# Optimization experiments

Measured on AMD Instinct MI355X. Metric: run time of the kernel, lower is better.

The kernel has to match this reference:

```python
import jax, jax.numpy as jnp
import numpy as np

HIDDEN = 2048
NUM_HEADS = 32
GROUP_SIZE = 4
HEAD_DIM = HIDDEN // NUM_HEADS            # 64
GROUP_NUM = NUM_HEADS // GROUP_SIZE       # 8 KV heads
B, S = 2, 2048


def setup_inputs() -> dict:
    key = jax.random.key(0)
    ks = jax.random.split(key, 7)
    sc = 1.0 / np.sqrt(HIDDEN)
    x = jax.random.normal(ks[0], (B, S, HIDDEN), dtype=jnp.float32)
    attention_mask = jnp.ones((B, S), dtype=jnp.int32)
    Wq = jax.random.normal(ks[1], (HIDDEN, HIDDEN), dtype=jnp.float32) * sc
    bq = jax.random.normal(ks[2], (HIDDEN,), dtype=jnp.float32) * 0.02
    Wk = jax.random.normal(ks[3], (HIDDEN, GROUP_NUM * HEAD_DIM), dtype=jnp.float32) * sc
    bk = jax.random.normal(ks[4], (GROUP_NUM * HEAD_DIM,), dtype=jnp.float32) * 0.02
    Wv = jax.random.normal(ks[5], (HIDDEN, GROUP_NUM * HEAD_DIM), dtype=jnp.float32) * sc
    bv = jax.random.normal(ks[6], (GROUP_NUM * HEAD_DIM,), dtype=jnp.float32) * 0.02
    return {"x": x, "attention_mask": attention_mask,
            "Wq": Wq, "bq": bq, "Wk": Wk, "bk": bk, "Wv": Wv, "bv": bv}


def reference(x, attention_mask, Wq, bq, Wk, bk, Wv, bv):
    b, s, _ = x.shape
    # projections
    q = (x @ Wq + bq).reshape(b, s, NUM_HEADS, HEAD_DIM).transpose(0, 2, 1, 3)   # (B,H,S,hd)
    k = (x @ Wk + bk).reshape(b, s, GROUP_NUM, HEAD_DIM).transpose(0, 2, 1, 3)   # (B,G,S,hd)
    v = (x @ Wv + bv).reshape(b, s, GROUP_NUM, HEAD_DIM).transpose(0, 2, 1, 3)
    # expand KV groups to full head count (head h uses group h // group_size)
    k = jnp.repeat(k, GROUP_SIZE, axis=1)                                        # (B,H,S,hd)
    v = jnp.repeat(v, GROUP_SIZE, axis=1)
    # NOTE: original torch code uses floor-division `//` for scaling and no softmax
    score = jnp.floor(jnp.einsum('bhqd,bhkd->bhqk', q, k) / np.sqrt(HEAD_DIM).astype(np.float32))
    score = jnp.where(attention_mask[:, None, None, :] == 0, -jnp.inf, score)
    out = jnp.einsum('bhqk,bhkd->bhqd', score, v)                                # (B,H,S,hd)
    return out.transpose(0, 2, 1, 3).reshape(b, s, HIDDEN)
```

## Files before the change

### kernel.cpp

```cpp
#include <hip/hip_runtime.h>
#include <math.h>

#define HIDDEN 2048
#define NHEADS 32
#define HDIM 64
#define GNUM 8
#define KVDIM 512
#define BB 2
#define SS 2048
#define MROWS (BB * SS)
#define NQKV 3072

typedef _Float16 half8 __attribute__((ext_vector_type(8)));
typedef _Float16 half4 __attribute__((ext_vector_type(4)));
typedef _Float16 half2 __attribute__((ext_vector_type(2)));
typedef float floatx4 __attribute__((ext_vector_type(4)));

#define MFMA16(a, b, c) __builtin_amdgcn_mfma_f32_16x16x32_f16((a), (b), (c), 0, 0, 0)

__device__ __forceinline__ void split_f32(float x, _Float16& hi, _Float16& lo) {
    hi = (_Float16)x;
    lo = (_Float16)((x - (float)hi) * 2048.0f);
}

__device__ __forceinline__ void load_lds16(const void* g, void* l) {
    __builtin_amdgcn_global_load_lds(
        (const __attribute__((address_space(1))) void*)g,
        (__attribute__((address_space(3))) void*)l, 16, 0, 0);
}

__global__ __launch_bounds__(256)
void split_x(const float* __restrict__ x, _Float16* __restrict__ xh,
             _Float16* __restrict__ xl, int n4) {
    for (int idx = blockIdx.x * 256 + threadIdx.x; idx < n4; idx += gridDim.x * 256) {
        floatx4 v = reinterpret_cast<const floatx4*>(x)[idx];
        half4 h, l;
        #pragma unroll
        for (int e = 0; e < 4; ++e) { _Float16 hi, lo; split_f32(v[e], hi, lo); h[e] = hi; l[e] = lo; }
        reinterpret_cast<half4*>(xh)[idx] = h;
        reinterpret_cast<half4*>(xl)[idx] = l;
    }
}

__global__ __launch_bounds__(256)
void split_wt(const float* __restrict__ W, int N, int n0,
              _Float16* __restrict__ Wth, _Float16* __restrict__ Wtl) {
    __shared__ float tile[64][68];
    const int tid = threadIdx.x;
    const int kb = blockIdx.x, nb = blockIdx.y;
    #pragma unroll
    for (int i = 0; i < 4; ++i) {
        int idx = tid + i * 256;
        int r = idx >> 4, c4 = idx & 15;
        floatx4 v = *reinterpret_cast<const floatx4*>(&W[(size_t)(kb * 64 + r) * N + nb * 64 + c4 * 4]);
        *reinterpret_cast<floatx4*>(&tile[r][c4 * 4]) = v;
    }
    __syncthreads();
    #pragma unroll
    for (int i = 0; i < 4; ++i) {
        int idx = tid + i * 256;
        int r2 = idx >> 4, c2 = (idx & 15) * 4;
        half4 h, l;
        #pragma unroll
        for (int e = 0; e < 4; ++e) {
            _Float16 hi, lo;
            split_f32(tile[c2 + e][r2], hi, lo);
            h[e] = hi; l[e] = lo;
        }
        size_t o = (size_t)(n0 + nb * 64 + r2) * HIDDEN + kb * 64 + c2;
        *reinterpret_cast<half4*>(&Wth[o]) = h;
        *reinterpret_cast<half4*>(&Wtl[o]) = l;
    }
}

__global__ __launch_bounds__(256)
void biascat_k(const float* __restrict__ bq, const float* __restrict__ bk,
               const float* __restrict__ bv, float* __restrict__ bias) {
    int i = blockIdx.x * 256 + threadIdx.x;
    if (i < 2048) bias[i] = bq[i];
    else if (i < 2560) bias[i] = bk[i - 2048];
    else if (i < NQKV) bias[i] = bv[i - 2560];
}

__global__ __launch_bounds__(256, 2)
void gemm_qkv(const _Float16* __restrict__ xh, const _Float16* __restrict__ xl,
              const _Float16* __restrict__ Wth, const _Float16* __restrict__ Wtl,
              const float* __restrict__ bias,
              _Float16* __restrict__ qh, _Float16* __restrict__ ql,
              _Float16* __restrict__ kh, _Float16* __restrict__ kl,
              _Float16* __restrict__ vh) {
    __shared__ __align__(16) _Float16 Ah[128 * 64];
    __shared__ __align__(16) _Float16 Al[128 * 64];
    __shared__ __align__(16) _Float16 Bh[128 * 64];
    __shared__ __align__(16) _Float16 Bl[128 * 64];

    const int tid  = threadIdx.x;
    const int lane = tid & 63;
    const int w    = tid >> 6;
    const int wm   = w >> 1, wn = w & 1;
    const int bm   = blockIdx.x, bn = blockIdx.y;
    const int ml   = lane & 15;
    const int kg8  = (lane >> 4) * 8;

    const _Float16* gsrc;
    _Float16* ldst;
    if      (w == 0) { gsrc = xh  + (size_t)(bm * 128) * HIDDEN; ldst = Ah; }
    else if (w == 1) { gsrc = xl  + (size_t)(bm * 128) * HIDDEN; ldst = Al; }
    else if (w == 2) { gsrc = Wth + (size_t)(bn * 128) * HIDDEN; ldst = Bh; }
    else             { gsrc = Wtl + (size_t)(bn * 128) * HIDDEN; ldst = Bl; }

    floatx4 acc0[4][4] = {};
    floatx4 accL[4][4] = {};

    for (int k0 = 0; k0 < HIDDEN; k0 += 64) {
        #pragma unroll
        for (int i = 0; i < 16; ++i) {
            int L   = i * 1024 + lane * 16;
            int row = L >> 7;
            int off = (L & 127) ^ ((row & 7) << 4);
            const void* gp = (const char*)(gsrc + (size_t)row * HIDDEN + k0) + off;
            void* lp = (char*)ldst + i * 1024;
            load_lds16(gp, lp);
        }
        __syncthreads();

        #pragma unroll
        for (int kc = 0; kc < 2; ++kc) {
            half8 a_h[4], a_l[4], b_h[4], b_l[4];
            #pragma unroll
            for (int r = 0; r < 4; ++r) {
                int row = wm * 64 + r * 16 + ml;
                int byt = row * 128 + (((kc * 64 + kg8 * 2)) ^ ((row & 7) << 4));
                a_h[r] = *reinterpret_cast<const half8*>((const char*)Ah + byt);
                a_l[r] = *reinterpret_cast<const half8*>((const char*)Al + byt);
            }
            #pragma unroll
            for (int c = 0; c < 4; ++c) {
                int row = wn * 64 + c * 16 + ml;
                int byt = row * 128 + (((kc * 64 + kg8 * 2)) ^ ((row & 7) << 4));
                b_h[c] = *reinterpret_cast<const half8*>((const char*)Bh + byt);
                b_l[c] = *reinterpret_cast<const half8*>((const char*)Bl + byt);
            }
            #pragma unroll
            for (int r = 0; r < 4; ++r)
                #pragma unroll
                for (int c = 0; c < 4; ++c) {
                    acc0[r][c] = MFMA16(a_h[r], b_h[c], acc0[r][c]);
                    accL[r][c] = MFMA16(a_h[r], b_l[c], accL[r][c]);
                    accL[r][c] = MFMA16(a_l[r], b_h[c], accL[r][c]);
                }
        }
        __syncthreads();
    }

    #pragma unroll
    for (int c = 0; c < 4; ++c) {
        int colg = bn * 128 + wn * 64 + c * 16 + ml;
        float bval = bias[colg];
        #pragma unroll
        for (int r = 0; r < 4; ++r) {
            int rowg = bm * 128 + wm * 64 + r * 16 + (lane >> 4) * 4;
            #pragma unroll
            for (int reg = 0; reg < 4; ++reg) {
                float val = acc0[r][c][reg] + accL[r][c][reg] * (1.0f / 2048.0f) + bval;
                int rr = rowg + reg;
                if (colg < 2048) {
                    _Float16 hi, lo; split_f32(val, hi, lo);
                    qh[(size_t)rr * HIDDEN + colg] = hi;
                    ql[(size_t)rr * HIDDEN + colg] = lo;
                } else if (colg < 2560) {
                    int ck = colg - 2048;
                    _Float16 hi, lo; split_f32(val, hi, lo);
                    kh[(size_t)rr * KVDIM + ck] = hi;
                    kl[(size_t)rr * KVDIM + ck] = lo;
                } else {
                    vh[(size_t)rr * KVDIM + (colg - 2560)] = (_Float16)val;
                }
            }
        }
    }
}

__global__ __launch_bounds__(256, 2)
void attn4(const _Float16* __restrict__ qh, const _Float16* __restrict__ ql,
           const _Float16* __restrict__ kh, const _Float16* __restrict__ kl,
           const _Float16* __restrict__ vh, const int* __restrict__ mask,
           float* __restrict__ out) {
    __shared__ __align__(16) _Float16 Ksh[64][72];
    __shared__ __align__(16) _Float16 Ksl[64][72];
    __shared__ __align__(16) _Float16 Vst[64][72];
    __shared__ __align__(16) _Float16 Ss[4][4][16][72];

    const int tid  = threadIdx.x;
    const int lane = tid & 63;
    const int w    = tid >> 6;
    const int ml   = lane & 15;
    const int kg8  = (lane >> 4) * 8;
    const int qt   = blockIdx.x;
    const int b    = blockIdx.y >> 3, g = blockIdx.y & 7;

    half8 qhf[4][2], qlf[4][2];
    {
        size_t rowbase = (size_t)(b * SS + qt * 64 + w * 16 + ml) * HIDDEN;
        #pragma unroll
        for (int hh = 0; hh < 4; ++hh) {
            int hcol = (g * 4 + hh) * HDIM;
            #pragma unroll
            for (int gch = 0; gch < 2; ++gch) {
                qhf[hh][gch] = *reinterpret_cast<const half8*>(&qh[rowbase + hcol + gch * 32 + kg8]);
                qlf[hh][gch] = *reinterpret_cast<const half8*>(&ql[rowbase + hcol + gch * 32 + kg8]);
            }
        }
    }

    const _Float16* khg = kh + (size_t)b * SS * KVDIM + g * HDIM;
    const _Float16* klg = kl + (size_t)b * SS * KVDIM + g * HDIM;
    const _Float16* vhg = vh + (size_t)b * SS * KVDIM + g * HDIM;
    const int* mb = mask + b * SS;

    floatx4 oacc[4][4] = {};

    for (int kt = 0; kt < SS / 64; ++kt) {
        __syncthreads();
        #pragma unroll
        for (int i = 0; i < 2; ++i) {
            int idx = tid + i * 256;
            int kk = idx >> 3, d8 = (idx & 7) * 8;
            *reinterpret_cast<half8*>(&Ksh[kk][d8]) =
                *reinterpret_cast<const half8*>(&khg[(size_t)(kt * 64 + kk) * KVDIM + d8]);
            *reinterpret_cast<half8*>(&Ksl[kk][d8]) =
                *reinterpret_cast<const half8*>(&klg[(size_t)(kt * 64 + kk) * KVDIM + d8]);
        }
        {
            int rp = (tid & 31) * 2, c8 = (tid >> 5) * 8;
            half8 v0 = *reinterpret_cast<const half8*>(&vhg[(size_t)(kt * 64 + rp) * KVDIM + c8]);
            half8 v1 = *reinterpret_cast<const half8*>(&vhg[(size_t)(kt * 64 + rp + 1) * KVDIM + c8]);
            #pragma unroll
            for (int e = 0; e < 8; ++e)
                *reinterpret_cast<half2*>(&Vst[c8 + e][rp]) = half2{v0[e], v1[e]};
        }
        __syncthreads();

        int mv[4];
        #pragma unroll
        for (int fc = 0; fc < 4; ++fc) mv[fc] = mb[kt * 64 + fc * 16 + ml];

        #pragma unroll
        for (int fc = 0; fc < 4; ++fc) {
            half8 k_h[2], k_l[2];
            #pragma unroll
            for (int gch = 0; gch < 2; ++gch) {
                k_h[gch] = *reinterpret_cast<const half8*>(&Ksh[fc * 16 + ml][gch * 32 + kg8]);
                k_l[gch] = *reinterpret_cast<const half8*>(&Ksl[fc * 16 + ml][gch * 32 + kg8]);
            }
            #pragma unroll
            for (int hh = 0; hh < 4; ++hh) {
                floatx4 s0 = {}, sL = {};
                #pragma unroll
                for (int gch = 0; gch < 2; ++gch) {
                    s0 = MFMA16(qhf[hh][gch], k_h[gch], s0);
                    sL = MFMA16(qhf[hh][gch], k_l[gch], sL);
                    sL = MFMA16(qlf[hh][gch], k_h[gch], sL);
                }
                #pragma unroll
                for (int r = 0; r < 4; ++r) {
                    float sv = s0[r] + sL[r] * (1.0f / 2048.0f);
                    sv = floorf(sv * 0.125f);
                    if (mv[fc] == 0) sv = -INFINITY;
                    Ss[w][hh][(lane >> 4) * 4 + r][fc * 16 + ml] = (_Float16)sv;
                }
            }
        }

        half8 sa[4][2];
        #pragma unroll
        for (int hh = 0; hh < 4; ++hh)
            #pragma unroll
            for (int sg = 0; sg < 2; ++sg)
                sa[hh][sg] = *reinterpret_cast<const half8*>(&Ss[w][hh][ml][sg * 32 + kg8]);
        #pragma unroll
        for (int f = 0; f < 4; ++f) {
            half8 vb0 = *reinterpret_cast<const half8*>(&Vst[f * 16 + ml][kg8]);
            half8 vb1 = *reinterpret_cast<const half8*>(&Vst[f * 16 + ml][32 + kg8]);
            #pragma unroll
            for (int hh = 0; hh < 4; ++hh) {
                oacc[hh][f] = MFMA16(sa[hh][0], vb0, oacc[hh][f]);
                oacc[hh][f] = MFMA16(sa[hh][1], vb1, oacc[hh][f]);
            }
        }
    }

    #pragma unroll
    for (int hh = 0; hh < 4; ++hh) {
        int hcol = (g * 4 + hh) * HDIM;
        #pragma unroll
        for (int f = 0; f < 4; ++f)
            #pragma unroll
            for (int reg = 0; reg < 4; ++reg) {
                int row = b * SS + qt * 64 + w * 16 + (lane >> 4) * 4 + reg;
                out[(size_t)row * HIDDEN + hcol + f * 16 + ml] = oacc[hh][f][reg];
            }
    }
}

extern "C" void kernel_launch(void* const* d_in, const int* in_sizes, int n_in,
                              void* d_out, int out_size, void* d_ws, size_t ws_size,
                              hipStream_t stream) {
    (void)in_sizes; (void)n_in; (void)out_size; (void)ws_size;
    const float* x    = (const float*)d_in[0];
    const int*   mask = (const int*)d_in[1];
    const float* Wq   = (const float*)d_in[2];
    const float* bq   = (const float*)d_in[3];
    const float* Wk   = (const float*)d_in[4];
    const float* bk   = (const float*)d_in[5];
    const float* Wv   = (const float*)d_in[6];
    const float* bv   = (const float*)d_in[7];

    _Float16* ws16 = (_Float16*)d_ws;
    size_t o = 0;
    auto alloc16 = [&](size_t n) { _Float16* p = ws16 + o; o += n; return p; };
    _Float16* xh  = alloc16((size_t)MROWS * HIDDEN);
    _Float16* xl  = alloc16((size_t)MROWS * HIDDEN);
    _Float16* Wth = alloc16((size_t)NQKV * HIDDEN);
    _Float16* Wtl = alloc16((size_t)NQKV * HIDDEN);
    _Float16* qh  = alloc16((size_t)MROWS * HIDDEN);
    _Float16* ql  = alloc16((size_t)MROWS * HIDDEN);
    _Float16* kh  = alloc16((size_t)MROWS * KVDIM);
    _Float16* kl  = alloc16((size_t)MROWS * KVDIM);
    _Float16* vh  = alloc16((size_t)MROWS * KVDIM);
    float* biascat = (float*)(ws16 + o);

    split_x<<<2048, 256, 0, stream>>>(x, xh, xl, MROWS * HIDDEN / 4);
    split_wt<<<dim3(32, 32), 256, 0, stream>>>(Wq, HIDDEN, 0,    Wth, Wtl);
    split_wt<<<dim3(32, 8),  256, 0, stream>>>(Wk, KVDIM, 2048, Wth, Wtl);
    split_wt<<<dim3(32, 8),  256, 0, stream>>>(Wv, KVDIM, 2560, Wth, Wtl);
    biascat_k<<<12, 256, 0, stream>>>(bq, bk, bv, biascat);
    gemm_qkv<<<dim3(MROWS / 128, NQKV / 128), 256, 0, stream>>>(
        xh, xl, Wth, Wtl, biascat, qh, ql, kh, kl, vh);
    attn4<<<dim3(SS / 64, BB * GNUM), 256, 0, stream>>>(qh, ql, kh, kl, vh, mask, (float*)d_out);
}
```

Baseline: 336.8 us.

## Keep attention scores in registers via permlane swaps and pre-swizzled K tiles

The GEMM epilogue now writes K hi/lo in a tiled, XOR-swizzled layout so the attention kernel can stream each 64x64 K tile straight into LDS with global_load_lds, and the padded LDS row layout is dropped. The score matrix no longer round-trips through shared memory. The QK product is computed transposed, packed to fp16 and rearranged with v_permlane32/16_swap so it can feed the PV MFMA directly as an operand. The 1/8 scale is folded into Q, the mask is read as int4, the output is written as vector stores, and the block index is remapped so blocks sharing a KV group run together. Pre-scaling Q in fp16 and the new swizzle and permute logic bring a risk of rounding or indexing errors.

Measured after the change: 305.6 us. 1.1x faster.

```diff
diff --git a/kernel.cpp b/kernel.cpp
--- a/kernel.cpp
+++ b/kernel.cpp
@@ -14,6 +14,7 @@
 typedef _Float16 half8 __attribute__((ext_vector_type(8)));
 typedef _Float16 half4 __attribute__((ext_vector_type(4)));
 typedef _Float16 half2 __attribute__((ext_vector_type(2)));
+typedef __fp16 fp16x2 __attribute__((ext_vector_type(2)));
 typedef float floatx4 __attribute__((ext_vector_type(4)));
 
 #define MFMA16(a, b, c) __builtin_amdgcn_mfma_f32_16x16x32_f16((a), (b), (c), 0, 0, 0)
@@ -27,6 +28,19 @@
     __builtin_amdgcn_global_load_lds(
         (const __attribute__((address_space(1))) void*)g,
         (__attribute__((address_space(3))) void*)l, 16, 0, 0);
+}
+
+__device__ __forceinline__ void permswap32(unsigned& a, unsigned& b) {
+    asm volatile("v_permlane32_swap_b32 %0, %1" : "+v"(a), "+v"(b));
+}
+__device__ __forceinline__ void permswap16(unsigned& a, unsigned& b) {
+    asm volatile("v_permlane16_swap_b32 %0, %1" : "+v"(a), "+v"(b));
+}
+
+__device__ __forceinline__ unsigned pk_f16(float a, float b) {
+    union { fp16x2 h; unsigned u; } c;
+    c.h = __builtin_amdgcn_cvt_pkrtz(a, b);
+    return c.u;
 }
 
 __global__ __launch_bounds__(256)
@@ -87,7 +101,7 @@
               const _Float16* __restrict__ Wth, const _Float16* __restrict__ Wtl,
               const float* __restrict__ bias,
               _Float16* __restrict__ qh, _Float16* __restrict__ ql,
-              _Float16* __restrict__ kh, _Float16* __restrict__ kl,
+              _Float16* __restrict__ khs, _Float16* __restrict__ kls,
               _Float16* __restrict__ vh) {
     __shared__ __align__(16) _Float16 Ah[128 * 64];
     __shared__ __align__(16) _Float16 Al[128 * 64];
@@ -170,9 +184,14 @@
                     ql[(size_t)rr * HIDDEN + colg] = lo;
                 } else if (colg < 2560) {
                     int ck = colg - 2048;
+                    int gk = ck >> 6, dk = ck & 63;
+                    int bk_ = rr >> 11, sk_ = rr & 2047;
+                    int kk = sk_ & 63;
+                    size_t baseK = ((size_t)((bk_ * 8 + gk) * 32 + (sk_ >> 6))) * 4096
+                                 + kk * 64 + (dk ^ ((kk & 7) << 3));
                     _Float16 hi, lo; split_f32(val, hi, lo);
-                    kh[(size_t)rr * KVDIM + ck] = hi;
-                    kl[(size_t)rr * KVDIM + ck] = lo;
+                    khs[baseK] = hi;
+                    kls[baseK] = lo;
                 } else {
                     vh[(size_t)rr * KVDIM + (colg - 2560)] = (_Float16)val;
                 }
@@ -182,22 +201,25 @@
 }
 
 __global__ __launch_bounds__(256, 2)
-void attn4(const _Float16* __restrict__ qh, const _Float16* __restrict__ ql,
-           const _Float16* __restrict__ kh, const _Float16* __restrict__ kl,
+void attn5(const _Float16* __restrict__ qh, const _Float16* __restrict__ ql,
+           const _Float16* __restrict__ khs, const _Float16* __restrict__ kls,
            const _Float16* __restrict__ vh, const int* __restrict__ mask,
            float* __restrict__ out) {
-    __shared__ __align__(16) _Float16 Ksh[64][72];
-    __shared__ __align__(16) _Float16 Ksl[64][72];
+    __shared__ __align__(16) _Float16 Ksh[64 * 64];
+    __shared__ __align__(16) _Float16 Ksl[64 * 64];
     __shared__ __align__(16) _Float16 Vst[64][72];
-    __shared__ __align__(16) _Float16 Ss[4][4][16][72];
 
     const int tid  = threadIdx.x;
     const int lane = tid & 63;
     const int w    = tid >> 6;
     const int ml   = lane & 15;
-    const int kg8  = (lane >> 4) * 8;
-    const int qt   = blockIdx.x;
-    const int b    = blockIdx.y >> 3, g = blockIdx.y & 7;
+    const int lg   = lane >> 4;
+    const int kg8  = lg * 8;
+
+    const int f_  = blockIdx.y * 32 + blockIdx.x;
+    const int bg  = (f_ & 7) | ((f_ >> 8) << 3);
+    const int qt  = (f_ >> 3) & 31;
+    const int b   = bg >> 3, g = bg & 7;
 
     half8 qhf[4][2], qlf[4][2];
     {
@@ -207,99 +229,115 @@
             int hcol = (g * 4 + hh) * HDIM;
             #pragma unroll
             for (int gch = 0; gch < 2; ++gch) {
-                qhf[hh][gch] = *reinterpret_cast<const half8*>(&qh[rowbase + hcol + gch * 32 + kg8]);
-                qlf[hh][gch] = *reinterpret_cast<const half8*>(&ql[rowbase + hcol + gch * 32 + kg8]);
-            }
-        }
-    }
-
-    const _Float16* khg = kh + (size_t)b * SS * KVDIM + g * HDIM;
-    const _Float16* klg = kl + (size_t)b * SS * KVDIM + g * HDIM;
-    const _Float16* vhg = vh + (size_t)b * SS * KVDIM + g * HDIM;
+                half8 a = *reinterpret_cast<const half8*>(&qh[rowbase + hcol + gch * 32 + kg8]);
+                half8 c = *reinterpret_cast<const half8*>(&ql[rowbase + hcol + gch * 32 + kg8]);
+                qhf[hh][gch] = a * (_Float16)0.125f;
+                qlf[hh][gch] = c * (_Float16)0.125f;
+            }
+        }
+    }
+
+    const _Float16* ktile_h = khs + (size_t)(bg * 32) * 4096;
+    const _Float16* ktile_l = kls + (size_t)(bg * 32) * 4096;
+    const _Float16* vbg = vh + (size_t)b * SS * KVDIM + g * HDIM;
     const int* mb = mask + b * SS;
 
     floatx4 oacc[4][4] = {};
 
     for (int kt = 0; kt < SS / 64; ++kt) {
         __syncthreads();
-        #pragma unroll
-        for (int i = 0; i < 2; ++i) {
-            int idx = tid + i * 256;
-            int kk = idx >> 3, d8 = (idx & 7) * 8;
-            *reinterpret_cast<half8*>(&Ksh[kk][d8]) =
-                *reinterpret_cast<const half8*>(&khg[(size_t)(kt * 64 + kk) * KVDIM + d8]);
-            *reinterpret_cast<half8*>(&Ksl[kk][d8]) =
-                *reinterpret_cast<const half8*>(&klg[(size_t)(kt * 64 + kk) * KVDIM + d8]);
+        if (w == 0) {
+            #pragma unroll
+            for (int j = 0; j < 8; ++j)
+                load_lds16((const char*)(ktile_h + (size_t)kt * 4096) + j * 1024 + lane * 16,
+                           (char*)Ksh + j * 1024);
+        } else if (w == 1) {
+            #pragma unroll
+            for (int j = 0; j < 8; ++j)
+                load_lds16((const char*)(ktile_l + (size_t)kt * 4096) + j * 1024 + lane * 16,
+                           (char*)Ksl + j * 1024);
         }
         {
             int rp = (tid & 31) * 2, c8 = (tid >> 5) * 8;
-            half8 v0 = *reinterpret_cast<const half8*>(&vhg[(size_t)(kt * 64 + rp) * KVDIM + c8]);
-            half8 v1 = *reinterpret_cast<const half8*>(&vhg[(size_t)(kt * 64 + rp + 1) * KVDIM + c8]);
+            half8 v0 = *reinterpret_cast<const half8*>(&vbg[(size_t)(kt * 64 + rp) * KVDIM + c8]);
+            half8 v1 = *reinterpret_cast<const half8*>(&vbg[(size_t)(kt * 64 + rp + 1) * KVDIM + c8]);
             #pragma unroll
             for (int e = 0; e < 8; ++e)
                 *reinterpret_cast<half2*>(&Vst[c8 + e][rp]) = half2{v0[e], v1[e]};
         }
         __syncthreads();
 
-        int mv[4];
-        #pragma unroll
-        for (int fc = 0; fc < 4; ++fc) mv[fc] = mb[kt * 64 + fc * 16 + ml];
-
+        half8 av[4][2];
+        #pragma unroll
+        for (int f = 0; f < 4; ++f)
+            #pragma unroll
+            for (int kc = 0; kc < 2; ++kc)
+                av[f][kc] = *reinterpret_cast<const half8*>(&Vst[f * 16 + ml][kc * 32 + kg8]);
+
+        int4 m4v[4];
+        #pragma unroll
+        for (int fc = 0; fc < 4; ++fc)
+            m4v[fc] = *reinterpret_cast<const int4*>(&mb[kt * 64 + fc * 16 + lg * 4]);
+
+        __builtin_amdgcn_s_setprio(1);
+
+        unsigned h2[4][4][2];
         #pragma unroll
         for (int fc = 0; fc < 4; ++fc) {
+            int krow = fc * 16 + ml;
+            int xo = (krow & 7) << 3;
             half8 k_h[2], k_l[2];
             #pragma unroll
             for (int gch = 0; gch < 2; ++gch) {
-                k_h[gch] = *reinterpret_cast<const half8*>(&Ksh[fc * 16 + ml][gch * 32 + kg8]);
-                k_l[gch] = *reinterpret_cast<const half8*>(&Ksl[fc * 16 + ml][gch * 32 + kg8]);
+                k_h[gch] = *reinterpret_cast<const half8*>(&Ksh[krow * 64 + ((gch * 32 + kg8) ^ xo)]);
+                k_l[gch] = *reinterpret_cast<const half8*>(&Ksl[krow * 64 + ((gch * 32 + kg8) ^ xo)]);
             }
             #pragma unroll
             for (int hh = 0; hh < 4; ++hh) {
-                floatx4 s0 = {}, sL = {};
-                #pragma unroll
-                for (int gch = 0; gch < 2; ++gch) {
-                    s0 = MFMA16(qhf[hh][gch], k_h[gch], s0);
-                    sL = MFMA16(qhf[hh][gch], k_l[gch], sL);
-                    sL = MFMA16(qlf[hh][gch], k_h[gch], sL);
-                }
+                floatx4 s0 = {}, sl = {};
+                s0 = MFMA16(k_h[0], qhf[hh][0], s0);
+                s0 = MFMA16(k_h[1], qhf[hh][1], s0);
+                sl = MFMA16(k_l[0], qhf[hh][0], sl);
+                sl = MFMA16(k_l[1], qhf[hh][1], sl);
+                sl = MFMA16(k_h[0], qlf[hh][0], sl);
+                sl = MFMA16(k_h[1], qlf[hh][1], sl);
+                float sv[4];
                 #pragma unroll
                 for (int r = 0; r < 4; ++r) {
-                    float sv = s0[r] + sL[r] * (1.0f / 2048.0f);
-                    sv = floorf(sv * 0.125f);
-                    if (mv[fc] == 0) sv = -INFINITY;
-                    Ss[w][hh][(lane >> 4) * 4 + r][fc * 16 + ml] = (_Float16)sv;
+                    float t = floorf(fmaf(sl[r], 1.0f / 2048.0f, s0[r]));
+                    sv[r] = (m4v[fc][r] == 0) ? -INFINITY : t;
                 }
-            }
-        }
-
-        half8 sa[4][2];
-        #pragma unroll
-        for (int hh = 0; hh < 4; ++hh)
-            #pragma unroll
-            for (int sg = 0; sg < 2; ++sg)
-                sa[hh][sg] = *reinterpret_cast<const half8*>(&Ss[w][hh][ml][sg * 32 + kg8]);
-        #pragma unroll
-        for (int f = 0; f < 4; ++f) {
-            half8 vb0 = *reinterpret_cast<const half8*>(&Vst[f * 16 + ml][kg8]);
-            half8 vb1 = *reinterpret_cast<const half8*>(&Vst[f * 16 + ml][32 + kg8]);
-            #pragma unroll
-            for (int hh = 0; hh < 4; ++hh) {
-                oacc[hh][f] = MFMA16(sa[hh][0], vb0, oacc[hh][f]);
-                oacc[hh][f] = MFMA16(sa[hh][1], vb1, oacc[hh][f]);
-            }
-        }
+                h2[hh][fc][0] = pk_f16(sv[0], sv[1]);
+                h2[hh][fc][1] = pk_f16(sv[2], sv[3]);
+            }
+        }
+
+        #pragma unroll
+        for (int hh = 0; hh < 4; ++hh) {
+            #pragma unroll
+            for (int kc = 0; kc < 2; ++kc) {
+                unsigned t0 = h2[hh][2 * kc][0], tA = h2[hh][2 * kc + 1][0];
+                unsigned t1 = h2[hh][2 * kc][1], tB = h2[hh][2 * kc + 1][1];
+                permswap32(t0, tA); permswap16(t0, tA);
+                permswap32(t1, tB); permswap16(t1, tB);
+                union { unsigned u[4]; half8 h; } bu;
+                bu.u[0] = t0; bu.u[1] = t1; bu.u[2] = tA; bu.u[3] = tB;
+                #pragma unroll
+                for (int f = 0; f < 4; ++f)
+                    oacc[hh][f] = MFMA16(av[f][kc], bu.h, oacc[hh][f]);
+            }
+        }
+        __builtin_amdgcn_s_setprio(0);
     }
 
     #pragma unroll
     for (int hh = 0; hh < 4; ++hh) {
         int hcol = (g * 4 + hh) * HDIM;
         #pragma unroll
-        for (int f = 0; f < 4; ++f)
-            #pragma unroll
-            for (int reg = 0; reg < 4; ++reg) {
-                int row = b * SS + qt * 64 + w * 16 + (lane >> 4) * 4 + reg;
-                out[(size_t)row * HIDDEN + hcol + f * 16 + ml] = oacc[hh][f][reg];
-            }
+        for (int f = 0; f < 4; ++f) {
+            size_t row = (size_t)(b * SS + qt * 64 + w * 16 + ml);
+            *reinterpret_cast<floatx4*>(&out[row * HIDDEN + hcol + f * 16 + lg * 4]) = oacc[hh][f];
+        }
     }
 }
 
@@ -325,8 +363,8 @@
     _Float16* Wtl = alloc16((size_t)NQKV * HIDDEN);
     _Float16* qh  = alloc16((size_t)MROWS * HIDDEN);
     _Float16* ql  = alloc16((size_t)MROWS * HIDDEN);
-    _Float16* kh  = alloc16((size_t)MROWS * KVDIM);
-    _Float16* kl  = alloc16((size_t)MROWS * KVDIM);
+    _Float16* khs = alloc16((size_t)MROWS * KVDIM);
+    _Float16* kls = alloc16((size_t)MROWS * KVDIM);
     _Float16* vh  = alloc16((size_t)MROWS * KVDIM);
     float* biascat = (float*)(ws16 + o);
 
@@ -336,6 +374,6 @@
     split_wt<<<dim3(32, 8),  256, 0, stream>>>(Wv, KVDIM, 2560, Wth, Wtl);
     biascat_k<<<12, 256, 0, stream>>>(bq, bk, bv, biascat);
     gemm_qkv<<<dim3(MROWS / 128, NQKV / 128), 256, 0, stream>>>(
-        xh, xl, Wth, Wtl, biascat, qh, ql, kh, kl, vh);
-    attn4<<<dim3(SS / 64, BB * GNUM), 256, 0, stream>>>(qh, ql, kh, kl, vh, mask, (float*)d_out);
-}
+        xh, xl, Wth, Wtl, biascat, qh, ql, khs, kls, vh);
+    attn5<<<dim3(32, 16), 256, 0, stream>>>(qh, ql, khs, kls, vh, mask, (float*)d_out);
+}
```
